# Performance work log

Measured on AMD Instinct MI355X. Metric: run time of the kernel, lower is better.

Reference implementation:

```python
import jax, jax.numpy as jnp
import numpy as np

W_LEN = 8      # window_len
DEPTH = 3      # sig_depth (implementation hardcodes depth-3 truncated signature)


def _seg_exp(d):
    """Truncated tensor-exponential of a linear segment with increment d (N,D)."""
    t1 = d
    t2 = 0.5 * jnp.einsum('ni,nj->nij', d, d)
    t3 = jnp.einsum('nij,nk->nijk', t2, d) / 3.0  # d^{\otimes 3}/6
    return t1, t2, t3


def _signature_depth3(path):
    """path: (N, L, D) -> flattened depth-3 signature (N, D + D^2 + D^3),
    matching signatory.signature ordering (levels concatenated, row-major)."""
    N, L, D = path.shape
    dx = path[:, 1:] - path[:, :-1]          # (N, L-1, D) increments
    s1, s2, s3 = _seg_exp(dx[:, 0])

    def chen_step(carry, d):
        s1, s2, s3 = carry
        t1, t2, t3 = _seg_exp(d)
        n1 = s1 + t1
        n2 = s2 + jnp.einsum('ni,nj->nij', s1, t1) + t2
        n3 = (s3
              + jnp.einsum('nij,nk->nijk', s2, t1)
              + jnp.einsum('ni,njk->nijk', s1, t2)
              + t3)
        return (n1, n2, n3), None

    # scan over the remaining L-2 increments (time axis leading)
    (s1, s2, s3), _ = jax.lax.scan(chen_step, (s1, s2, s3),
                                   jnp.moveaxis(dx[:, 1:], 1, 0))
    return jnp.concatenate([s1, s2.reshape(N, -1), s3.reshape(N, -1)], axis=-1)


def _rolling_windows(x, w_len):
    """x: (B,T,D) -> (B,T,W,D); window t covers [max(0,t-W+1), t],
    left-padded by repeating the first element (clamped indices)."""
    T = x.shape[1]
    idx = jnp.clip(jnp.arange(T)[:, None] - (w_len - 1) + jnp.arange(w_len)[None, :], 0, T - 1)  # (T,W)
    return x[:, idx]  # (B,T,W,D)


def setup_inputs() -> dict:
    key = jax.random.key(0)
    k1, k2, k3 = jax.random.split(key, 3)
    B, T, D = 8, 4096, 8
    sig_channels = D + D * D + D * D * D  # 584
    proj_dim = 128
    x = jax.random.normal(k1, (B, T, D), dtype=jnp.float32)
    w_proj = jax.random.normal(k2, (sig_channels, proj_dim), dtype=jnp.float32) * (1.0 / np.sqrt(sig_channels))
    b_proj = jax.random.normal(k3, (proj_dim,), dtype=jnp.float32) * 0.01
    return {"x": x, "w_proj": w_proj, "b_proj": b_proj}


def reference(x, w_proj, b_proj):
    B, T, D = x.shape
    windows = _rolling_windows(x, W_LEN).reshape(B * T, W_LEN, D)
    sig = _signature_depth3(windows).reshape(B, T, -1)   # (B,T,584)
    return sig @ w_proj + b_proj                          # (B,T,128)
```

## Files before the change

### kernel.cpp

```cpp
#include <hip/hip_runtime.h>
#include <hip/hip_bf16.h>

typedef unsigned short ushort_t;
typedef __attribute__((ext_vector_type(8))) short short8;
typedef __attribute__((ext_vector_type(4))) float floatx4;
typedef __attribute__((ext_vector_type(4))) int intx4;

#define SIG_CH 584
#define KPAD   608
#define NKB    76
#define NPROJ  128
#define ASTRIDE 616
#define TLEN   4096
#define NWIN   32768
#define DROWS  4103
#define WPB    32

__device__ __forceinline__ ushort_t f2bf(float f) {
    unsigned int v; __builtin_memcpy(&v, &f, 4);
    v += 0x7fffu + ((v >> 16) & 1u);
    return (ushort_t)(v >> 16);
}

__global__ void pack_kernel(const float* __restrict__ w, const float* __restrict__ x,
                            ushort_t* __restrict__ wp, float* __restrict__ dincP) {
    int idx = blockIdx.x * 256 + threadIdx.x;
    if (idx < KPAD * NPROJ) {
        int n = idx & (NPROJ - 1);
        int c = idx >> 7;
        ushort_t v = 0;
        if (c < SIG_CH) v = f2bf(w[c * NPROJ + n]);
        wp[((size_t)(c >> 3) * NPROJ + n) * 8 + (c & 7)] = v;
        return;
    }
    int id2 = idx - KPAD * NPROJ;
    if (id2 >= 8 * DROWS * 8) return;
    int k  = id2 & 7;
    int rr = (id2 >> 3) % DROWS;
    int b  = (id2 >> 3) / DROWS;
    float v = 0.f;
    if (rr >= 8) {
        int ta = rr - 8;
        const float* xb = x + (size_t)b * TLEN * 8;
        v = xb[(ta + 1) * 8 + k] - xb[ta * 8 + k];
    }
    dincP[((size_t)b * DROWS + rr) * 8 + k] = v;
}

__launch_bounds__(256, 3)
__global__ void sig_gemm_kernel(const float* __restrict__ dincP,
                                const ushort_t* __restrict__ wp,
                                const float* __restrict__ bias,
                                float* __restrict__ out) {
    __shared__ float    s_dinc[WPB + 6][8];
    __shared__ ushort_t s_A[WPB][ASTRIDE];

    const int tid  = threadIdx.x;
    const int blk  = blockIdx.x;
    const int g0   = blk * WPB;
    const int b    = g0 >> 12;
    const int t0   = g0 & (TLEN - 1);
    const float* dincB = dincP + (size_t)b * DROWS * 8;

    if (tid < (WPB + 6) * 2) {
        ((floatx4*)s_dinc)[tid] =
            *(const floatx4*)(dincB + (size_t)(t0 + 1) * 8 + tid * 4);
    }
    for (int idx = tid; idx < WPB * 32; idx += 256) {
        int r = idx >> 5, c = SIG_CH + (idx & 31);
        s_A[r][c] = 0;
    }
    __syncthreads();

    const int wv   = tid >> 6;
    const int lane = tid & 63;
    const int li   = lane >> 3;
    const int lj   = lane & 7;

    #pragma unroll 1
    for (int ww = 0; ww < 8; ++ww) {
        const int w = wv * 8 + ww;
        const int  woff = __builtin_amdgcn_readfirstlane((t0 + 1 + w) * 8);
        const float* dw = dincB + woff;

        float h = 0.f, g = 0.f, s2 = 0.f;
        float s3[8] = {0.f, 0.f, 0.f, 0.f, 0.f, 0.f, 0.f, 0.f};
        #pragma unroll
        for (int st = 0; st < 7; ++st) {
            const float di = s_dinc[w + st][li];
            const float dj = s_dinc[w + st][lj];
            const float c3 = fmaf(dj, fmaf(0.166666667f, di, 0.5f * h), s2);
            s2 = fmaf(dj, fmaf(0.5f, di, h), s2);
            #pragma unroll
            for (int k = 0; k < 8; ++k)
                s3[k] = fmaf(c3, dw[st * 8 + k], s3[k]);
            h += di;
            g += dj;
        }
        union { ushort_t u[8]; intx4 v; } pk;
        #pragma unroll
        for (int k = 0; k < 8; ++k) pk.u[k] = f2bf(s3[k]);
        *(intx4*)(&s_A[w][72 + lane * 8]) = pk.v;
        s_A[w][8 + lane] = f2bf(s2);
        if (lane < 8) s_A[w][lane] = f2bf(g);
    }
    __syncthreads();

    const int lrow  = lane & 15;
    const int kgrp  = lane >> 4;
    const int ncol0 = wv * 32 + lrow;

    floatx4 acc[2][2];
    #pragma unroll
    for (int mt = 0; mt < 2; ++mt) {
        acc[mt][0] = floatx4{0.f, 0.f, 0.f, 0.f};
        acc[mt][1] = floatx4{0.f, 0.f, 0.f, 0.f};
    }

    for (int kc = 0; kc < 19; ++kc) {
        const int kb = kc * 4 + kgrp;
        const short8 b0 = *(const short8*)(wp + ((size_t)kb * NPROJ + ncol0) * 8);
        const short8 b1 = *(const short8*)(wp + ((size_t)kb * NPROJ + ncol0 + 16) * 8);
        #pragma unroll
        for (int mt = 0; mt < 2; ++mt) {
            const short8 af = *(const short8*)(&s_A[mt * 16 + lrow][kc * 32 + kgrp * 8]);
            acc[mt][0] = __builtin_amdgcn_mfma_f32_16x16x32_bf16(af, b0, acc[mt][0], 0, 0, 0);
            acc[mt][1] = __builtin_amdgcn_mfma_f32_16x16x32_bf16(af, b1, acc[mt][1], 0, 0, 0);
        }
    }

    const float bias0 = bias[ncol0];
    const float bias1 = bias[ncol0 + 16];
    #pragma unroll
    for (int mt = 0; mt < 2; ++mt) {
        #pragma unroll
        for (int r = 0; r < 4; ++r) {
            const int row = g0 + mt * 16 + kgrp * 4 + r;
            out[(size_t)row * NPROJ + ncol0]      = acc[mt][0][r] + bias0;
            out[(size_t)row * NPROJ + ncol0 + 16] = acc[mt][1][r] + bias1;
        }
    }
}

extern "C" void kernel_launch(void* const* d_in, const int* in_sizes, int n_in,
                              void* d_out, int out_size, void* d_ws, size_t ws_size,
                              hipStream_t stream) {
    const float* x  = (const float*)d_in[0];
    const float* w  = (const float*)d_in[1];
    const float* bp = (const float*)d_in[2];
    ushort_t* wp    = (ushort_t*)d_ws;
    float*    dincP = (float*)((char*)d_ws + 160 * 1024);
    float* out = (float*)d_out;

    const int prep_total = KPAD * NPROJ + 8 * DROWS * 8;
    hipLaunchKernelGGL(pack_kernel, dim3((prep_total + 255) / 256), dim3(256), 0, stream,
                       w, x, wp, dincP);
    hipLaunchKernelGGL(sig_gemm_kernel, dim3(NWIN / WPB), dim3(256), 0, stream,
                       dincP, wp, bp, out);
}
```

Baseline: 75.23 us.

## Compute increments in-kernel from x and cache window rows in registers

Removes the padded increment buffer from the pre-pass: the main kernel now loads x directly and computes increments into shared memory, including a transposed copy. Each wave preloads its per-lane di/dj sequences and a rotating set of 7 increment rows into registers, which replaces repeated global loads of dw and shared loads inside the signature loop. The window loop is fully unrolled. Register pressure rises under the 3-blocks-per-CU launch bound, which could cause spills.

```diff
diff --git a/kernel.cpp b/kernel.cpp
--- a/kernel.cpp
+++ b/kernel.cpp
@@ -4,17 +4,17 @@
 typedef unsigned short ushort_t;
 typedef __attribute__((ext_vector_type(8))) short short8;
 typedef __attribute__((ext_vector_type(4))) float floatx4;
+typedef __attribute__((ext_vector_type(2))) float floatx2;
 typedef __attribute__((ext_vector_type(4))) int intx4;
 
 #define SIG_CH 584
 #define KPAD   608
-#define NKB    76
 #define NPROJ  128
 #define ASTRIDE 616
 #define TLEN   4096
 #define NWIN   32768
-#define DROWS  4103
 #define WPB    32
+#define TSTR   40
 
 __device__ __forceinline__ ushort_t f2bf(float f) {
     unsigned int v; __builtin_memcpy(&v, &f, 4);
@@ -22,37 +22,23 @@
     return (ushort_t)(v >> 16);
 }
 
-__global__ void pack_kernel(const float* __restrict__ w, const float* __restrict__ x,
-                            ushort_t* __restrict__ wp, float* __restrict__ dincP) {
+__global__ void pack_w_kernel(const float* __restrict__ w, ushort_t* __restrict__ wp) {
     int idx = blockIdx.x * 256 + threadIdx.x;
-    if (idx < KPAD * NPROJ) {
-        int n = idx & (NPROJ - 1);
-        int c = idx >> 7;
-        ushort_t v = 0;
-        if (c < SIG_CH) v = f2bf(w[c * NPROJ + n]);
-        wp[((size_t)(c >> 3) * NPROJ + n) * 8 + (c & 7)] = v;
-        return;
-    }
-    int id2 = idx - KPAD * NPROJ;
-    if (id2 >= 8 * DROWS * 8) return;
-    int k  = id2 & 7;
-    int rr = (id2 >> 3) % DROWS;
-    int b  = (id2 >> 3) / DROWS;
-    float v = 0.f;
-    if (rr >= 8) {
-        int ta = rr - 8;
-        const float* xb = x + (size_t)b * TLEN * 8;
-        v = xb[(ta + 1) * 8 + k] - xb[ta * 8 + k];
-    }
-    dincP[((size_t)b * DROWS + rr) * 8 + k] = v;
+    if (idx >= KPAD * NPROJ) return;
+    int n = idx & (NPROJ - 1);
+    int c = idx >> 7;
+    ushort_t v = 0;
+    if (c < SIG_CH) v = f2bf(w[c * NPROJ + n]);
+    wp[((size_t)(c >> 3) * NPROJ + n) * 8 + (c & 7)] = v;
 }
 
 __launch_bounds__(256, 3)
-__global__ void sig_gemm_kernel(const float* __restrict__ dincP,
+__global__ void sig_gemm_kernel(const float* __restrict__ x,
                                 const ushort_t* __restrict__ wp,
                                 const float* __restrict__ bias,
                                 float* __restrict__ out) {
     __shared__ float    s_dinc[WPB + 6][8];
+    __shared__ float    s_dincT[8][TSTR];
     __shared__ ushort_t s_A[WPB][ASTRIDE];
 
     const int tid  = threadIdx.x;
@@ -60,11 +46,21 @@
     const int g0   = blk * WPB;
     const int b    = g0 >> 12;
     const int t0   = g0 & (TLEN - 1);
-    const float* dincB = dincP + (size_t)b * DROWS * 8;
 
     if (tid < (WPB + 6) * 2) {
-        ((floatx4*)s_dinc)[tid] =
-            *(const floatx4*)(dincB + (size_t)(t0 + 1) * 8 + tid * 4);
+        const int s    = tid >> 1;
+        const int half = tid & 1;
+        const int ta   = t0 - 7 + s;
+        floatx4 d4 = floatx4{0.f, 0.f, 0.f, 0.f};
+        if (ta >= 0) {
+            const float* p = x + ((size_t)b * TLEN + ta) * 8 + half * 4;
+            const floatx4 a0 = *(const floatx4*)p;
+            const floatx4 a1 = *(const floatx4*)(p + 8);
+            d4 = a1 - a0;
+        }
+        *(floatx4*)(&s_dinc[s][half * 4]) = d4;
+        #pragma unroll
+        for (int l = 0; l < 4; ++l) s_dincT[half * 4 + l][s] = d4[l];
     }
     for (int idx = tid; idx < WPB * 32; idx += 256) {
         int r = idx >> 5, c = SIG_CH + (idx & 31);
@@ -76,24 +72,49 @@
     const int lane = tid & 63;
     const int li   = lane >> 3;
     const int lj   = lane & 7;
+    const int w0   = wv * 8;
 
-    #pragma unroll 1
+    float dis[14], djs[14];
+    {
+        const float* pi = &s_dincT[li][w0];
+        const float* pj = &s_dincT[lj][w0];
+        *(floatx4*)&dis[0] = *(const floatx4*)(pi);
+        *(floatx4*)&dis[4] = *(const floatx4*)(pi + 4);
+        *(floatx4*)&dis[8] = *(const floatx4*)(pi + 8);
+        *(floatx2*)&dis[12] = *(const floatx2*)(pi + 12);
+        *(floatx4*)&djs[0] = *(const floatx4*)(pj);
+        *(floatx4*)&djs[4] = *(const floatx4*)(pj + 4);
+        *(floatx4*)&djs[8] = *(const floatx4*)(pj + 8);
+        *(floatx2*)&djs[12] = *(const floatx2*)(pj + 12);
+    }
+
+    float rows[7][8];
+    #pragma unroll
+    for (int r = 0; r < 6; ++r) {
+        *(floatx4*)&rows[r][0] = *(const floatx4*)&s_dinc[w0 + r][0];
+        *(floatx4*)&rows[r][4] = *(const floatx4*)&s_dinc[w0 + r][4];
+    }
+
+    #pragma unroll
     for (int ww = 0; ww < 8; ++ww) {
-        const int w = wv * 8 + ww;
-        const int  woff = __builtin_amdgcn_readfirstlane((t0 + 1 + w) * 8);
-        const float* dw = dincB + woff;
-
+        const int w = w0 + ww;
+        {
+            const int slot = (ww + 6) % 7;
+            *(floatx4*)&rows[slot][0] = *(const floatx4*)&s_dinc[w + 6][0];
+            *(floatx4*)&rows[slot][4] = *(const floatx4*)&s_dinc[w + 6][4];
+        }
         float h = 0.f, g = 0.f, s2 = 0.f;
         float s3[8] = {0.f, 0.f, 0.f, 0.f, 0.f, 0.f, 0.f, 0.f};
         #pragma unroll
         for (int st = 0; st < 7; ++st) {
-            const float di = s_dinc[w + st][li];
-            const float dj = s_dinc[w + st][lj];
+            const float* d = rows[(ww + st) % 7];
+            const float di = dis[ww + st];
+            const float dj = djs[ww + st];
             const float c3 = fmaf(dj, fmaf(0.166666667f, di, 0.5f * h), s2);
             s2 = fmaf(dj, fmaf(0.5f, di, h), s2);
             #pragma unroll
             for (int k = 0; k < 8; ++k)
-                s3[k] = fmaf(c3, dw[st * 8 + k], s3[k]);
+                s3[k] = fmaf(c3, d[k], s3[k]);
             h += di;
             g += dj;
         }
@@ -149,12 +170,10 @@
     const float* w  = (const float*)d_in[1];
     const float* bp = (const float*)d_in[2];
     ushort_t* wp    = (ushort_t*)d_ws;
-    float*    dincP = (float*)((char*)d_ws + 160 * 1024);
     float* out = (float*)d_out;
 
-    const int prep_total = KPAD * NPROJ + 8 * DROWS * 8;
-    hipLaunchKernelGGL(pack_kernel, dim3((prep_total + 255) / 256), dim3(256), 0, stream,
-                       w, x, wp, dincP);
+    hipLaunchKernelGGL(pack_w_kernel, dim3((KPAD * NPROJ + 255) / 256), dim3(256), 0, stream,
+                       w, wp);
     hipLaunchKernelGGL(sig_gemm_kernel, dim3(NWIN / WPB), dim3(256), 0, stream,
-                       dincP, wp, bp, out);
+                       x, wp, bp, out);
 }
```

After: 75.68 us. Within noise of the previous version (+0.6%).
